# Performance work log

Measured on AMD Instinct MI355X. Metric: run time of the kernel, lower is better.

Reference implementation:

```python
import jax, jax.numpy as jnp
import numpy as np

N, E, D_IN, D_H, N_CLS, N_GRAPHS = 50000, 1600000, 128, 64, 10, 64
NEG_SLOPE = 0.2


def _glorot(key, shape):
    fan_in = shape[0]
    return (jax.random.normal(key, shape, dtype=jnp.float32) * np.sqrt(1.0 / fan_in)).astype(jnp.float32)


def setup_inputs() -> dict:
    key = jax.random.key(0)
    ks = jax.random.split(key, 20)
    inp = {
        "x": jax.random.normal(ks[0], (N, D_IN), dtype=jnp.float32),
        "edge_index": jax.random.randint(ks[1], (2, E), 0, N, dtype=jnp.int64) if jax.config.jax_enable_x64 else jax.random.randint(ks[1], (2, E), 0, N).astype(jnp.int32),
        "edge_attr": jax.random.uniform(ks[2], (E, 1), dtype=jnp.float32),
        "batch": jnp.sort(jax.random.randint(ks[3], (N,), 0, N_GRAPHS)),
        # conv1 params
        "Wl1": _glorot(ks[4], (D_IN, D_H)), "bl1": jnp.zeros((D_H,), jnp.float32),
        "Wr1": _glorot(ks[5], (D_IN, D_H)), "br1": jnp.zeros((D_H,), jnp.float32),
        "We1": _glorot(ks[6], (1, D_H)),
        "att1": _glorot(ks[7], (D_H,)),
        "b1": jnp.zeros((D_H,), jnp.float32),
        # conv2 params
        "Wl2": _glorot(ks[8], (D_H, D_H)), "bl2": jnp.zeros((D_H,), jnp.float32),
        "Wr2": _glorot(ks[9], (D_H, D_H)), "br2": jnp.zeros((D_H,), jnp.float32),
        "We2": _glorot(ks[10], (1, D_H)),
        "att2": _glorot(ks[11], (D_H,)),
        "b2": jnp.zeros((D_H,), jnp.float32),
        # classifier
        "Wc": _glorot(ks[12], (D_H, N_CLS)), "bc": jnp.zeros((N_CLS,), jnp.float32),
    }
    return inp


def _segment_softmax(logits, seg, num_segments):
    m = jax.ops.segment_max(logits, seg, num_segments=num_segments)
    z = jnp.exp(logits - m[seg])
    s = jax.ops.segment_sum(z, seg, num_segments=num_segments)
    return z / (s[seg] + 1e-16)


def _gatv2(x, src, dst, eattr, Wl, bl, Wr, br, We, att, b):
    # PyG GATv2Conv, heads=1, add_self_loops=True (fill_value='mean'), eval mode
    xl = x @ Wl + bl  # source-side transform [N, D]
    xr = x @ Wr + br  # target-side transform [N, D]
    loop = jnp.arange(N, dtype=src.dtype)
    src2 = jnp.concatenate([src, loop])
    dst2 = jnp.concatenate([dst, loop])
    loop_attr = jnp.broadcast_to(eattr.mean(axis=0, keepdims=True), (N, eattr.shape[1]))
    ea2 = jnp.concatenate([eattr, loop_attr], axis=0) @ We  # [E+N, D]
    msg = jax.nn.leaky_relu(xl[src2] + xr[dst2] + ea2, NEG_SLOPE)  # [E+N, D]
    logits = msg @ att  # [E+N]
    alpha = _segment_softmax(logits, dst2, N)
    out = jax.ops.segment_sum(xl[src2] * alpha[:, None], dst2, num_segments=N)
    return out + b


def reference(x, edge_index, edge_attr, batch,
              Wl1, bl1, Wr1, br1, We1, att1, b1,
              Wl2, bl2, Wr2, br2, We2, att2, b2,
              Wc, bc):
    src, dst = edge_index[0], edge_index[1]
    h = jax.nn.elu(_gatv2(x, src, dst, edge_attr, Wl1, bl1, Wr1, br1, We1, att1, b1))
    # dropout p=0.2 is identity in eval mode
    h = jax.nn.elu(_gatv2(h, src, dst, edge_attr, Wl2, bl2, Wr2, br2, We2, att2, b2))
    # global mean pool per graph
    sums = jax.ops.segment_sum(h, batch, num_segments=N_GRAPHS)
    counts = jax.ops.segment_sum(jnp.ones((N,), h.dtype), batch, num_segments=N_GRAPHS)
    pooled = sums / jnp.maximum(counts, 1.0)[:, None]  # [G, D_H]
    return pooled @ Wc + bc
```

## Files before the change

### kernel.cpp

```cpp
#include <hip/hip_runtime.h>
#include <hip/hip_fp16.h>
#include <math.h>

#define N_NODES 50000
#define N_EDGES 1600000
#define D_IN 128
#define D_H 64
#define N_CLS 10
#define N_GRAPHS 64
#define NEG_SLOPE 0.2f
#define E2 (N_EDGES + N_NODES)
#define SCAN_BS 256
#define NBLK ((N_NODES + SCAN_BS - 1) / SCAN_BS)

#define NB 25
#define BSH 11
#define CAP 76800
#define HBB 8
#define EPT 8
#define PAD 32
#define SLICES 8
#define SLICE_W (2048 / SLICES)

typedef _Float16 f16x2 __attribute__((ext_vector_type(2)));

__device__ inline f16x2 as_h2(unsigned u) { return __builtin_bit_cast(f16x2, u); }
__device__ inline int h2_as_int(f16x2 v) { return __builtin_bit_cast(int, v); }

__device__ inline f16x2 pk_leaky(f16x2 m, f16x2 ns) {
#if __has_builtin(__builtin_elementwise_max)
    return __builtin_elementwise_max(m, m * ns);
#else
    f16x2 p = m * ns, r;
    r.x = m.x > p.x ? m.x : p.x;
    r.y = m.y > p.y ? m.y : p.y;
    return r;
#endif
}

#if __has_builtin(__builtin_amdgcn_fdot2)
__device__ inline float fdot2a(f16x2 a, f16x2 b, float c) {
    return __builtin_amdgcn_fdot2(a, b, c, false);
}
#else
__device__ inline float fdot2a(f16x2 a, f16x2 b, float c) {
    return fmaf((float)a.x, (float)b.x, fmaf((float)a.y, (float)b.y, c));
}
#endif

__device__ inline float wave_reduce_sum(float v) {
    for (int off = 32; off; off >>= 1) v += __shfl_xor(v, off);
    return v;
}

__global__ void bucket_stage(const int* __restrict__ src, const int* __restrict__ dst,
                             const float* __restrict__ eattr,
                             float* esum, int* bcursor,
                             int2* __restrict__ stg) {
    __shared__ int bcnt[4][32];
    __shared__ int woff[4][32];
    __shared__ float esh[4];
    int t = threadIdx.x;
    int wave = t >> 6;
    if (t < 128) bcnt[t >> 5][t & 31] = 0;
    __syncthreads();
    int e0 = (blockIdx.x * blockDim.x + t) * EPT;
    int ss[EPT], tt[EPT], aa[EPT], r[EPT], b[EPT];
    float v = 0.f;
    bool valid = e0 < N_EDGES;
    if (valid) {
        #pragma unroll
        for (int q = 0; q < EPT / 4; ++q) {
            int4 s4 = *(const int4*)(src + e0 + 4 * q);
            int4 t4 = *(const int4*)(dst + e0 + 4 * q);
            float4 a4 = *(const float4*)(eattr + e0 + 4 * q);
            ss[4*q] = s4.x; ss[4*q+1] = s4.y; ss[4*q+2] = s4.z; ss[4*q+3] = s4.w;
            tt[4*q] = t4.x; tt[4*q+1] = t4.y; tt[4*q+2] = t4.z; tt[4*q+3] = t4.w;
            aa[4*q]   = h2_as_int((f16x2){(_Float16)a4.x, (_Float16)a4.x});
            aa[4*q+1] = h2_as_int((f16x2){(_Float16)a4.y, (_Float16)a4.y});
            aa[4*q+2] = h2_as_int((f16x2){(_Float16)a4.z, (_Float16)a4.z});
            aa[4*q+3] = h2_as_int((f16x2){(_Float16)a4.w, (_Float16)a4.w});
            v += (a4.x + a4.y) + (a4.z + a4.w);
        }
        #pragma unroll
        for (int i = 0; i < EPT; ++i) {
            b[i] = tt[i] >> BSH;
            r[i] = atomicAdd(&bcnt[wave][b[i]], 1);
        }
    }
    v = wave_reduce_sum(v);
    if ((t & 63) == 0) esh[wave] = v;
    __syncthreads();
    if (t < NB) {
        int c0 = bcnt[0][t], c1 = bcnt[1][t], c2 = bcnt[2][t], c3 = bcnt[3][t];
        int tot = c0 + c1 + c2 + c3;
        int base = tot ? atomicAdd(&bcursor[t * PAD], tot) : 0;
        woff[0][t] = base;
        woff[1][t] = base + c0;
        woff[2][t] = base + c0 + c1;
        woff[3][t] = base + c0 + c1 + c2;
    }
    if (t == 0) {
        float tot = (esh[0] + esh[1]) + (esh[2] + esh[3]);
        atomicAdd(&esum[(blockIdx.x & 31) * PAD], tot);
    }
    __syncthreads();
    if (valid) {
        #pragma unroll
        for (int i = 0; i < EPT; ++i) {
            int p = b[i] * CAP + woff[wave][b[i]] + r[i];
            stg[p] = make_int2((ss[i] & 0xFFFF) | ((tt[i] & 2047) << 16), aa[i]);
        }
    }
}

__global__ void hist_bucket(const int2* __restrict__ stg, const int* __restrict__ bcursor,
                            int* cnt) {
    __shared__ int hist[2048];
    int b = blockIdx.x / HBB;
    int j = blockIdx.x % HBB;
    for (int i = threadIdx.x; i < 2048; i += 256) hist[i] = 0;
    __syncthreads();
    int n = bcursor[b * PAD];
    const int2* sd = stg + (size_t)b * CAP;
    int per = (n + HBB - 1) / HBB;
    int start = j * per;
    int end = min(start + per, n);
    for (int idx = start + threadIdx.x; idx < end; idx += 256)
        atomicAdd(&hist[(sd[idx].x >> 16) & 2047], 1);
    __syncthreads();
    int nb = b << BSH;
    for (int i = threadIdx.x; i < 2048; i += 256) {
        int c = hist[i];
        if (c) atomicAdd(&cnt[nb + i], c);
    }
}

__global__ void scan_block(const int* __restrict__ cnt, int* __restrict__ row_start,
                           int* __restrict__ partial) {
    __shared__ int sd[SCAN_BS];
    int i = blockIdx.x * SCAN_BS + threadIdx.x;
    int v = (i < N_NODES) ? (cnt[i] + 1) : 0;
    sd[threadIdx.x] = v;
    __syncthreads();
    for (int off = 1; off < SCAN_BS; off <<= 1) {
        int t = (threadIdx.x >= off) ? sd[threadIdx.x - off] : 0;
        __syncthreads();
        sd[threadIdx.x] += t;
        __syncthreads();
    }
    if (i < N_NODES) row_start[i] = sd[threadIdx.x] - v;
    if (threadIdx.x == SCAN_BS - 1) partial[blockIdx.x] = sd[threadIdx.x];
}
__global__ void add_offsets(int* __restrict__ row_start, const int* __restrict__ partial,
                            int* __restrict__ cursor, const float* __restrict__ esum,
                            int2* __restrict__ csr_pack) {
    __shared__ int sp[SCAN_BS];
    int pv = (threadIdx.x < NBLK) ? partial[threadIdx.x] : 0;
    sp[threadIdx.x] = pv;
    __syncthreads();
    for (int off = 1; off < SCAN_BS; off <<= 1) {
        int t = (threadIdx.x >= off) ? sp[threadIdx.x - off] : 0;
        __syncthreads();
        sp[threadIdx.x] += t;
        __syncthreads();
    }
    float es = 0.f;
    #pragma unroll
    for (int jj = 0; jj < 32; ++jj) es += esum[jj * PAD];
    float esm = es * (1.0f / N_EDGES);
    int ebits = h2_as_int((f16x2){(_Float16)esm, (_Float16)esm});
    int base = (blockIdx.x == 0) ? 0 : sp[blockIdx.x - 1];
    int i = blockIdx.x * SCAN_BS + threadIdx.x;
    if (i < N_NODES) {
        int r = row_start[i] + base;
        row_start[i] = r;
        csr_pack[r] = make_int2(i, ebits);
        cursor[i] = r + 1;
    }
    if (i == 0) row_start[N_NODES] = E2;
}

__global__ __launch_bounds__(1024) void scatter_slice(
                              const int2* __restrict__ stg,
                              const int* __restrict__ bcursor,
                              const int* __restrict__ row_start,
                              int2* __restrict__ csr_pack) {
    __shared__ int lcur[SLICE_W];
    int b = blockIdx.x & 31;
    int m = blockIdx.x >> 5;
    if (b >= NB) return;
    int nbase = (b << BSH) + m * SLICE_W;
    for (int i = threadIdx.x; i < SLICE_W; i += 1024) {
        int node = nbase + i;
        lcur[i] = (node < N_NODES) ? row_start[node] + 1 : 0;
    }
    __syncthreads();
    int n = bcursor[b * PAD];
    const int4* sd4 = (const int4*)(stg + (size_t)b * CAP);
    int n4 = n >> 1;
    int lo = m * SLICE_W, hi = lo + SLICE_W;
    for (int base4 = 0; base4 < n4; base4 += 4096) {
        int4 e[4];
        int idx[4];
        #pragma unroll
        for (int j = 0; j < 4; ++j) {
            idx[j] = base4 + j * 1024 + (int)threadIdx.x;
            if (idx[j] < n4) e[j] = sd4[idx[j]];
        }
        #pragma unroll
        for (int j = 0; j < 4; ++j) {
            if (idx[j] < n4) {
                int dl0 = (e[j].x >> 16) & 2047;
                if (dl0 >= lo && dl0 < hi) {
                    int q = atomicAdd(&lcur[dl0 - lo], 1);
                    csr_pack[q] = make_int2(e[j].x & 0xFFFF, e[j].y);
                }
                int dl1 = (e[j].z >> 16) & 2047;
                if (dl1 >= lo && dl1 < hi) {
                    int q = atomicAdd(&lcur[dl1 - lo], 1);
                    csr_pack[q] = make_int2(e[j].z & 0xFFFF, e[j].w);
                }
            }
        }
    }
    if ((n & 1) && threadIdx.x == 0) {
        int2 e = stg[(size_t)b * CAP + n - 1];
        int dl = (e.x >> 16) & 2047;
        if (dl >= lo && dl < hi) {
            int q = atomicAdd(&lcur[dl - lo], 1);
            csr_pack[q] = make_int2(e.x & 0xFFFF, e.y);
        }
    }
}

template<int K>
__global__ __launch_bounds__(256) void linear_dual_k(
                              const float* __restrict__ x,
                              const float* __restrict__ Wl, const float* __restrict__ bl,
                              const float* __restrict__ Wr, const float* __restrict__ br,
                              __half* __restrict__ xl, __half* __restrict__ xr) {
    const int TN = 32;
    const int NPW = TN / 4;
    __shared__ float xs[TN * K];
    int t = threadIdx.x;
    int nb = blockIdx.x * TN;
    int rem = N_NODES - nb;
    int tot4 = (rem >= TN ? TN : rem) * (K / 4);
    const float4* xg = (const float4*)(x + (size_t)nb * K);
    float4* xs4 = (float4*)xs;
    for (int i = t; i < tot4; i += 256) xs4[i] = xg[i];
    __syncthreads();
    int wave = t >> 6, d = t & 63;
    int n0 = wave * NPW;
    float blv = bl[d], brv = br[d];
    float al[NPW], ar[NPW];
    #pragma unroll
    for (int i = 0; i < NPW; ++i) { al[i] = blv; ar[i] = brv; }
    #pragma unroll 2
    for (int k4 = 0; k4 < K / 4; ++k4) {
        int kb = k4 * 4;
        float wl[4], wr[4];
        #pragma unroll
        for (int q = 0; q < 4; ++q) {
            wl[q] = Wl[(kb + q) * D_H + d];
            wr[q] = Wr[(kb + q) * D_H + d];
        }
        #pragma unroll
        for (int i = 0; i < NPW; ++i) {
            float4 xv = *(const float4*)&xs[(n0 + i) * K + kb];
            al[i] = fmaf(xv.x, wl[0], al[i]);
            al[i] = fmaf(xv.y, wl[1], al[i]);
            al[i] = fmaf(xv.z, wl[2], al[i]);
            al[i] = fmaf(xv.w, wl[3], al[i]);
            ar[i] = fmaf(xv.x, wr[0], ar[i]);
            ar[i] = fmaf(xv.y, wr[1], ar[i]);
            ar[i] = fmaf(xv.z, wr[2], ar[i]);
            ar[i] = fmaf(xv.w, wr[3], ar[i]);
        }
    }
    #pragma unroll
    for (int i = 0; i < NPW; ++i) {
        int g = nb + n0 + i;
        if (g < N_NODES) {
            xl[(size_t)g * D_H + d] = __float2half(al[i]);
            xr[(size_t)g * D_H + d] = __float2half(ar[i]);
        }
    }
}

__global__ __launch_bounds__(256) void gat_fused(
        const int* __restrict__ row_start, const int2* __restrict__ csr_pack,
        const __half* __restrict__ xl, const __half* __restrict__ xr,
        const float* __restrict__ We, const float* __restrict__ att,
        const float* __restrict__ b, float* __restrict__ out) {
    int lane = threadIdx.x & 63;
    int g = lane >> 3;
    int s = lane & 7;
    int wid = blockIdx.x * (blockDim.x >> 6) + (threadIdx.x >> 6);
    int node = wid * 8 + g;
    bool nv = node < N_NODES;
    int nodec = nv ? node : 0;
    int fb = s * 8;
    float4 wea = *(const float4*)(We + fb), web = *(const float4*)(We + fb + 4);
    float4 ata = *(const float4*)(att + fb), atb = *(const float4*)(att + fb + 4);
    f16x2 we[4] = {{(_Float16)wea.x, (_Float16)wea.y}, {(_Float16)wea.z, (_Float16)wea.w},
                   {(_Float16)web.x, (_Float16)web.y}, {(_Float16)web.z, (_Float16)web.w}};
    f16x2 at[4] = {{(_Float16)ata.x, (_Float16)ata.y}, {(_Float16)ata.z, (_Float16)ata.w},
                   {(_Float16)atb.x, (_Float16)atb.y}, {(_Float16)atb.z, (_Float16)atb.w}};
    int4 xru = *(const int4*)(xr + (size_t)nodec * D_H + fb);
    f16x2 xr4[4] = {as_h2((unsigned)xru.x), as_h2((unsigned)xru.y),
                    as_h2((unsigned)xru.z), as_h2((unsigned)xru.w)};
    const f16x2 ns = {(_Float16)NEG_SLOPE, (_Float16)NEG_SLOPE};
    int j0 = 0, j1 = 0;
    if (nv) { j0 = row_start[node]; j1 = row_start[node + 1]; }

    float S = 0.f;
    float acc[8] = {0.f, 0.f, 0.f, 0.f, 0.f, 0.f, 0.f, 0.f};

    for (int i0 = j0; i0 < j1; i0 += 4) {
        int2 pk[4]; int4 qk[4]; bool vk[4];
        #pragma unroll
        for (int k = 0; k < 4; ++k) {
            vk[k] = (i0 + k) < j1;
            int c = vk[k] ? (i0 + k) : i0;
            pk[k] = csr_pack[c];
        }
        #pragma unroll
        for (int k = 0; k < 4; ++k)
            qk[k] = *(const int4*)(xl + (size_t)pk[k].x * D_H + fb);
        float t[4];
        #pragma unroll
        for (int k = 0; k < 4; ++k) {
            f16x2 a2 = as_h2((unsigned)pk[k].y);
            f16x2 r0 = as_h2((unsigned)qk[k].x), r1 = as_h2((unsigned)qk[k].y);
            f16x2 r2 = as_h2((unsigned)qk[k].z), r3 = as_h2((unsigned)qk[k].w);
            f16x2 m0 = a2 * we[0] + (r0 + xr4[0]);
            f16x2 m1 = a2 * we[1] + (r1 + xr4[1]);
            f16x2 m2 = a2 * we[2] + (r2 + xr4[2]);
            f16x2 m3 = a2 * we[3] + (r3 + xr4[3]);
            m0 = pk_leaky(m0, ns); m1 = pk_leaky(m1, ns);
            m2 = pk_leaky(m2, ns); m3 = pk_leaky(m3, ns);
            t[k] = fdot2a(m3, at[3], fdot2a(m2, at[2],
                   fdot2a(m1, at[1], fdot2a(m0, at[0], 0.f))));
        }
        #pragma unroll
        for (int off = 1; off <= 4; off <<= 1) {
            t[0] += __shfl_xor(t[0], off);
            t[1] += __shfl_xor(t[1], off);
            t[2] += __shfl_xor(t[2], off);
            t[3] += __shfl_xor(t[3], off);
        }
        #pragma unroll
        for (int k = 0; k < 4; ++k) {
            float z = vk[k] ? __expf(t[k]) : 0.f;
            S += z;
            f16x2 r0 = as_h2((unsigned)qk[k].x), r1 = as_h2((unsigned)qk[k].y);
            f16x2 r2 = as_h2((unsigned)qk[k].z), r3 = as_h2((unsigned)qk[k].w);
            acc[0] = fmaf(z, (float)r0.x, acc[0]);
            acc[1] = fmaf(z, (float)r0.y, acc[1]);
            acc[2] = fmaf(z, (float)r1.x, acc[2]);
            acc[3] = fmaf(z, (float)r1.y, acc[3]);
            acc[4] = fmaf(z, (float)r2.x, acc[4]);
            acc[5] = fmaf(z, (float)r2.y, acc[5]);
            acc[6] = fmaf(z, (float)r3.x, acc[6]);
            acc[7] = fmaf(z, (float)r3.y, acc[7]);
        }
    }

    if (nv) {
        float4 ba = *(const float4*)(b + fb), bb = *(const float4*)(b + fb + 4);
        float bq[8] = {ba.x, ba.y, ba.z, ba.w, bb.x, bb.y, bb.z, bb.w};
        float inv = 1.f / (S + 1e-16f);
        float h[8];
        #pragma unroll
        for (int j = 0; j < 8; ++j) {
            float v = fmaf(acc[j], inv, bq[j]);
            h[j] = v > 0.f ? v : expm1f(v);
        }
        *(float4*)(out + (size_t)node * D_H + fb)     = make_float4(h[0], h[1], h[2], h[3]);
        *(float4*)(out + (size_t)node * D_H + fb + 4) = make_float4(h[4], h[5], h[6], h[7]);
    }
}

__global__ void pool(const float* __restrict__ h, const int* __restrict__ batch,
                     float* __restrict__ pooled, float* __restrict__ counts) {
    const int CHUNK = 32;
    int base = blockIdx.x * CHUNK;
    int d = threadIdx.x;
    float accv = 0.f; int cur_g = -1; int cnt = 0;
    for (int i = 0; i < CHUNK; ++i) {
        int n = base + i;
        if (n >= N_NODES) break;
        int g = batch[n];
        if (g != cur_g) {
            if (cur_g >= 0) {
                atomicAdd(&pooled[cur_g * D_H + d], accv);
                if (d == 0) atomicAdd(&counts[cur_g], (float)cnt);
            }
            cur_g = g; accv = 0.f; cnt = 0;
        }
        accv += h[(size_t)n * D_H + d];
        cnt++;
    }
    if (cur_g >= 0) {
        atomicAdd(&pooled[cur_g * D_H + d], accv);
        if (d == 0) atomicAdd(&counts[cur_g], (float)cnt);
    }
}

__global__ void classify(const float* __restrict__ pooled, const float* __restrict__ counts,
                         const float* __restrict__ Wc, const float* __restrict__ bc,
                         float* __restrict__ out) {
    int tid = threadIdx.x;
    int g = tid / N_CLS, c = tid % N_CLS;
    if (g >= N_GRAPHS) return;
    float inv = 1.0f / fmaxf(counts[g], 1.0f);
    float a = bc[c];
    for (int k = 0; k < D_H; ++k)
        a = fmaf(pooled[g * D_H + k] * inv, Wc[k * N_CLS + c], a);
    out[g * N_CLS + c] = a;
}

extern "C" void kernel_launch(void* const* d_in, const int* in_sizes, int n_in,
                              void* d_out, int out_size, void* d_ws, size_t ws_size,
                              hipStream_t stream) {
    const float* x     = (const float*)d_in[0];
    const int*   ei    = (const int*)d_in[1];
    const float* eattr = (const float*)d_in[2];
    const int*   batch = (const int*)d_in[3];
    const float *Wl1 = (const float*)d_in[4],  *bl1 = (const float*)d_in[5];
    const float *Wr1 = (const float*)d_in[6],  *br1 = (const float*)d_in[7];
    const float *We1 = (const float*)d_in[8],  *att1 = (const float*)d_in[9];
    const float *b1  = (const float*)d_in[10];
    const float *Wl2 = (const float*)d_in[11], *bl2 = (const float*)d_in[12];
    const float *Wr2 = (const float*)d_in[13], *br2 = (const float*)d_in[14];
    const float *We2 = (const float*)d_in[15], *att2 = (const float*)d_in[16];
    const float *b2  = (const float*)d_in[17];
    const float *Wc  = (const float*)d_in[18], *bc = (const float*)d_in[19];
    float* out = (float*)d_out;

    const int* src = ei;
    const int* dst = ei + N_EDGES;

    char* base = (char*)d_ws;
    int2*  stg     = (int2*)base;
    __half* xl     = (__half*)base;
    __half* xr     = xl + (size_t)N_NODES * D_H;
    float* h       = (float*)(xr + (size_t)N_NODES * D_H);
    int2*  csr_pack = (int2*)(base + (size_t)NB * CAP * 16);
    int*   row_start = (int*)(csr_pack + E2);
    int*   cnt     = row_start + N_NODES + 1;
    float* esum    = (float*)(cnt + N_NODES);
    int*   bcursor = (int*)(esum + 32 * PAD);
    int*   cursor  = bcursor + NB * PAD;
    int*   partial = cursor + N_NODES;
    float* pooled  = (float*)(partial + NBLK);
    float* counts  = pooled + N_GRAPHS * D_H;

    int gat_blocks = (N_NODES + 31) / 32;
    int lin_blocks = (N_NODES + 31) / 32;

    hipMemsetAsync(cnt, 0, (N_NODES + 32 * PAD + NB * PAD) * sizeof(int), stream);
    hipMemsetAsync(pooled, 0, (N_GRAPHS * D_H + N_GRAPHS) * sizeof(float), stream);

    bucket_stage<<<(N_EDGES / EPT + 255) / 256, 256, 0, stream>>>(
        src, dst, eattr, esum, bcursor, stg);
    hist_bucket<<<NB * HBB, 256, 0, stream>>>(stg, bcursor, cnt);
    scan_block<<<NBLK, SCAN_BS, 0, stream>>>(cnt, row_start, partial);
    add_offsets<<<NBLK, SCAN_BS, 0, stream>>>(row_start, partial, cursor, esum, csr_pack);
    scatter_slice<<<SLICES * 32, 1024, 0, stream>>>(stg, bcursor, row_start, csr_pack);

    linear_dual_k<D_IN><<<lin_blocks, 256, 0, stream>>>(x, Wl1, bl1, Wr1, br1, xl, xr);
    gat_fused<<<gat_blocks, 256, 0, stream>>>(row_start, csr_pack, xl, xr, We1, att1, b1, h);

    linear_dual_k<D_H><<<lin_blocks, 256, 0, stream>>>(h, Wl2, bl2, Wr2, br2, xl, xr);
    gat_fused<<<gat_blocks, 256, 0, stream>>>(row_start, csr_pack, xl, xr, We2, att2, b2, h);

    pool<<<(N_NODES + 31) / 32, 64, 0, stream>>>(h, batch, pooled, counts);
    classify<<<1, 640, 0, stream>>>(pooled, counts, Wc, bc, out);
}
```

Measured before the change: 333.8 us.

## Sort nodes by in-degree to balance GAT wavefront work

Adds a degree histogram, scan and placement pass that produces a node order grouped by in-degree, and makes the GAT aggregation kernel process nodes in that order. Each wavefront handles eight nodes at once, so grouping nodes of similar degree is meant to cut idle lanes from divergent loop trip counts. The cost is three extra small kernel launches, an indirect node lookup, and scattered output and xr accesses in place of contiguous ones. Degrees are Poisson around 33 here, so the imbalance being removed is modest.

Measured after the change: 343.5 us. 2.9% more time.

```diff
diff --git a/kernel.cpp b/kernel.cpp
--- a/kernel.cpp
+++ b/kernel.cpp
@@ -21,6 +21,7 @@
 #define PAD 32
 #define SLICES 8
 #define SLICE_W (2048 / SLICES)
+#define DBINS 128
 
 typedef _Float16 f16x2 __attribute__((ext_vector_type(2)));
 
@@ -179,6 +180,59 @@
         cursor[i] = r + 1;
     }
     if (i == 0) row_start[N_NODES] = E2;
+}
+
+__global__ void deg_hist(const int* __restrict__ row_start, int* __restrict__ dbin) {
+    __shared__ int lh[DBINS];
+    int t = threadIdx.x;
+    for (int i = t; i < DBINS; i += 256) lh[i] = 0;
+    __syncthreads();
+    int i = blockIdx.x * 256 + t;
+    if (i < N_NODES) {
+        int d = min(row_start[i + 1] - row_start[i], DBINS - 1);
+        atomicAdd(&lh[d], 1);
+    }
+    __syncthreads();
+    for (int j = t; j < DBINS; j += 256) {
+        int c = lh[j];
+        if (c) atomicAdd(&dbin[j * PAD], c);
+    }
+}
+__global__ void deg_scan(const int* __restrict__ dbin, int* __restrict__ dcur) {
+    __shared__ int sd[DBINS];
+    int t = threadIdx.x;
+    int v = dbin[t * PAD];
+    sd[t] = v;
+    __syncthreads();
+    for (int off = 1; off < DBINS; off <<= 1) {
+        int u = (t >= off) ? sd[t - off] : 0;
+        __syncthreads();
+        sd[t] += u;
+        __syncthreads();
+    }
+    dcur[t * PAD] = sd[t] - v;
+}
+__global__ void deg_place(const int* __restrict__ row_start, int* __restrict__ dcur,
+                          int* __restrict__ order) {
+    __shared__ int lh[DBINS];
+    __shared__ int lbase[DBINS];
+    int t = threadIdx.x;
+    for (int i = t; i < DBINS; i += 256) lh[i] = 0;
+    __syncthreads();
+    int i = blockIdx.x * 256 + t;
+    int d = 0, r = 0;
+    bool v = i < N_NODES;
+    if (v) {
+        d = min(row_start[i + 1] - row_start[i], DBINS - 1);
+        r = atomicAdd(&lh[d], 1);
+    }
+    __syncthreads();
+    for (int j = t; j < DBINS; j += 256) {
+        int c = lh[j];
+        lbase[j] = c ? atomicAdd(&dcur[j * PAD], c) : 0;
+    }
+    __syncthreads();
+    if (v) order[lbase[d] + r] = i;
 }
 
 __global__ __launch_bounds__(1024) void scatter_slice(
@@ -291,6 +345,7 @@
 
 __global__ __launch_bounds__(256) void gat_fused(
         const int* __restrict__ row_start, const int2* __restrict__ csr_pack,
+        const int* __restrict__ order,
         const __half* __restrict__ xl, const __half* __restrict__ xr,
         const float* __restrict__ We, const float* __restrict__ att,
         const float* __restrict__ b, float* __restrict__ out) {
@@ -298,9 +353,9 @@
     int g = lane >> 3;
     int s = lane & 7;
     int wid = blockIdx.x * (blockDim.x >> 6) + (threadIdx.x >> 6);
-    int node = wid * 8 + g;
-    bool nv = node < N_NODES;
-    int nodec = nv ? node : 0;
+    int idx = wid * 8 + g;
+    bool nv = idx < N_NODES;
+    int node = nv ? order[idx] : 0;
     int fb = s * 8;
     float4 wea = *(const float4*)(We + fb), web = *(const float4*)(We + fb + 4);
     float4 ata = *(const float4*)(att + fb), atb = *(const float4*)(att + fb + 4);
@@ -308,7 +363,7 @@
                    {(_Float16)web.x, (_Float16)web.y}, {(_Float16)web.z, (_Float16)web.w}};
     f16x2 at[4] = {{(_Float16)ata.x, (_Float16)ata.y}, {(_Float16)ata.z, (_Float16)ata.w},
                    {(_Float16)atb.x, (_Float16)atb.y}, {(_Float16)atb.z, (_Float16)atb.w}};
-    int4 xru = *(const int4*)(xr + (size_t)nodec * D_H + fb);
+    int4 xru = *(const int4*)(xr + (size_t)node * D_H + fb);
     f16x2 xr4[4] = {as_h2((unsigned)xru.x), as_h2((unsigned)xru.y),
                     as_h2((unsigned)xru.z), as_h2((unsigned)xru.w)};
     const f16x2 ns = {(_Float16)NEG_SLOPE, (_Float16)NEG_SLOPE};
@@ -323,7 +378,7 @@
         #pragma unroll
         for (int k = 0; k < 4; ++k) {
             vk[k] = (i0 + k) < j1;
-            int c = vk[k] ? (i0 + k) : i0;
+            int c = vk[k] ? (i0 + k) : j0;
             pk[k] = csr_pack[c];
         }
         #pragma unroll
@@ -457,25 +512,32 @@
     int*   partial = cursor + N_NODES;
     float* pooled  = (float*)(partial + NBLK);
     float* counts  = pooled + N_GRAPHS * D_H;
+    int*   dbin    = (int*)(counts + N_GRAPHS);
+    int*   dcur    = dbin + DBINS * PAD;
+    int*   order   = dcur + DBINS * PAD;
 
     int gat_blocks = (N_NODES + 31) / 32;
     int lin_blocks = (N_NODES + 31) / 32;
 
     hipMemsetAsync(cnt, 0, (N_NODES + 32 * PAD + NB * PAD) * sizeof(int), stream);
-    hipMemsetAsync(pooled, 0, (N_GRAPHS * D_H + N_GRAPHS) * sizeof(float), stream);
+    hipMemsetAsync(pooled, 0,
+                   (N_GRAPHS * D_H + N_GRAPHS + DBINS * PAD) * sizeof(float), stream);
 
     bucket_stage<<<(N_EDGES / EPT + 255) / 256, 256, 0, stream>>>(
         src, dst, eattr, esum, bcursor, stg);
     hist_bucket<<<NB * HBB, 256, 0, stream>>>(stg, bcursor, cnt);
     scan_block<<<NBLK, SCAN_BS, 0, stream>>>(cnt, row_start, partial);
     add_offsets<<<NBLK, SCAN_BS, 0, stream>>>(row_start, partial, cursor, esum, csr_pack);
+    deg_hist<<<NBLK, 256, 0, stream>>>(row_start, dbin);
+    deg_scan<<<1, DBINS, 0, stream>>>(dbin, dcur);
+    deg_place<<<NBLK, 256, 0, stream>>>(row_start, dcur, order);
     scatter_slice<<<SLICES * 32, 1024, 0, stream>>>(stg, bcursor, row_start, csr_pack);
 
     linear_dual_k<D_IN><<<lin_blocks, 256, 0, stream>>>(x, Wl1, bl1, Wr1, br1, xl, xr);
-    gat_fused<<<gat_blocks, 256, 0, stream>>>(row_start, csr_pack, xl, xr, We1, att1, b1, h);
+    gat_fused<<<gat_blocks, 256, 0, stream>>>(row_start, csr_pack, order, xl, xr, We1, att1, b1, h);
 
     linear_dual_k<D_H><<<lin_blocks, 256, 0, stream>>>(h, Wl2, bl2, Wr2, br2, xl, xr);
-    gat_fused<<<gat_blocks, 256, 0, stream>>>(row_start, csr_pack, xl, xr, We2, att2, b2, h);
+    gat_fused<<<gat_blocks, 256, 0, stream>>>(row_start, csr_pack, order, xl, xr, We2, att2, b2, h);
 
     pool<<<(N_NODES + 31) / 32, 64, 0, stream>>>(h, batch, pooled, counts);
     classify<<<1, 640, 0, stream>>>(pooled, counts, Wc, bc, out);
```

## Compute dual node linear transforms with fp16 MFMA instructions

Applied to the files above, without the earlier changes.

Replaces the scalar-FMA dual linear kernel with one that converts a 64-node tile of inputs and transposed Wl/Wr weights to fp16 in shared memory. Each wave then computes the outputs for 16 nodes with 16x16x16 f16 MFMA instructions, one accumulator per 16-column tile of the combined 128 outputs. This cuts ALU work in the dense projections, but every block reloads and converts the full weight matrices, and the inputs lose precision from fp32 to fp16.

Result: faster. 307.9 us (-7.8%).

```diff
diff --git a/kernel.cpp b/kernel.cpp
--- a/kernel.cpp
+++ b/kernel.cpp
@@ -23,6 +23,8 @@
 #define SLICE_W (2048 / SLICES)
 
 typedef _Float16 f16x2 __attribute__((ext_vector_type(2)));
+typedef _Float16 f16x4 __attribute__((ext_vector_type(4)));
+typedef float    fv4   __attribute__((ext_vector_type(4)));
 
 __device__ inline f16x2 as_h2(unsigned u) { return __builtin_bit_cast(f16x2, u); }
 __device__ inline int h2_as_int(f16x2 v) { return __builtin_bit_cast(int, v); }
@@ -235,57 +237,92 @@
 }
 
 template<int K>
-__global__ __launch_bounds__(256) void linear_dual_k(
-                              const float* __restrict__ x,
-                              const float* __restrict__ Wl, const float* __restrict__ bl,
-                              const float* __restrict__ Wr, const float* __restrict__ br,
-                              __half* __restrict__ xl, __half* __restrict__ xr) {
-    const int TN = 32;
-    const int NPW = TN / 4;
-    __shared__ float xs[TN * K];
+__global__ __launch_bounds__(256) void linear_dual_mfma(
+        const float* __restrict__ x,
+        const float* __restrict__ Wl, const float* __restrict__ bl,
+        const float* __restrict__ Wr, const float* __restrict__ br,
+        __half* __restrict__ xl, __half* __restrict__ xr) {
+    const int KS = K + 4;
+    __shared__ _Float16 Xh[64 * KS];
+    __shared__ _Float16 Wt[128 * KS];
     int t = threadIdx.x;
-    int nb = blockIdx.x * TN;
-    int rem = N_NODES - nb;
-    int tot4 = (rem >= TN ? TN : rem) * (K / 4);
-    const float4* xg = (const float4*)(x + (size_t)nb * K);
-    float4* xs4 = (float4*)xs;
-    for (int i = t; i < tot4; i += 256) xs4[i] = xg[i];
-    __syncthreads();
-    int wave = t >> 6, d = t & 63;
-    int n0 = wave * NPW;
-    float blv = bl[d], brv = br[d];
-    float al[NPW], ar[NPW];
-    #pragma unroll
-    for (int i = 0; i < NPW; ++i) { al[i] = blv; ar[i] = brv; }
-    #pragma unroll 2
-    for (int k4 = 0; k4 < K / 4; ++k4) {
-        int kb = k4 * 4;
-        float wl[4], wr[4];
-        #pragma unroll
-        for (int q = 0; q < 4; ++q) {
-            wl[q] = Wl[(kb + q) * D_H + d];
-            wr[q] = Wr[(kb + q) * D_H + d];
-        }
-        #pragma unroll
-        for (int i = 0; i < NPW; ++i) {
-            float4 xv = *(const float4*)&xs[(n0 + i) * K + kb];
-            al[i] = fmaf(xv.x, wl[0], al[i]);
-            al[i] = fmaf(xv.y, wl[1], al[i]);
-            al[i] = fmaf(xv.z, wl[2], al[i]);
-            al[i] = fmaf(xv.w, wl[3], al[i]);
-            ar[i] = fmaf(xv.x, wr[0], ar[i]);
-            ar[i] = fmaf(xv.y, wr[1], ar[i]);
-            ar[i] = fmaf(xv.z, wr[2], ar[i]);
-            ar[i] = fmaf(xv.w, wr[3], ar[i]);
-        }
-    }
-    #pragma unroll
-    for (int i = 0; i < NPW; ++i) {
-        int g = nb + n0 + i;
-        if (g < N_NODES) {
-            xl[(size_t)g * D_H + d] = __float2half(al[i]);
-            xr[(size_t)g * D_H + d] = __float2half(ar[i]);
-        }
+    int nb = blockIdx.x * 64;
+    for (int i = t; i < 64 * (K / 4); i += 256) {
+        int n = i / (K / 4), k0 = (i % (K / 4)) * 4;
+        float4 v = (nb + n < N_NODES) ? *(const float4*)(x + (size_t)(nb + n) * K + k0)
+                                      : make_float4(0.f, 0.f, 0.f, 0.f);
+        f16x4 h = {(_Float16)v.x, (_Float16)v.y, (_Float16)v.z, (_Float16)v.w};
+        *(f16x4*)&Xh[n * KS + k0] = h;
+    }
+    for (int i = t; i < K * 64; i += 256) {
+        int k = i >> 6, c = i & 63;
+        Wt[c * KS + k] = (_Float16)Wl[i];
+    }
+    for (int i = t; i < K * 64; i += 256) {
+        int k = i >> 6, c = i & 63;
+        Wt[(c + 64) * KS + k] = (_Float16)Wr[i];
+    }
+    __syncthreads();
+
+    int w = t >> 6, lane = t & 63;
+    int np = lane & 15;
+    int g  = lane >> 4;
+    int node = nb + w * 16 + np;
+    const _Float16* xrow = &Xh[(w * 16 + np) * KS];
+    fv4 acc0 = {0.f,0.f,0.f,0.f}, acc1 = {0.f,0.f,0.f,0.f};
+    fv4 acc2 = {0.f,0.f,0.f,0.f}, acc3 = {0.f,0.f,0.f,0.f};
+    fv4 acc4 = {0.f,0.f,0.f,0.f}, acc5 = {0.f,0.f,0.f,0.f};
+    fv4 acc6 = {0.f,0.f,0.f,0.f}, acc7 = {0.f,0.f,0.f,0.f};
+
+#if __has_builtin(__builtin_amdgcn_mfma_f32_16x16x16f16)
+    for (int k0 = 0; k0 < K; k0 += 16) {
+        f16x4 bf = *(const f16x4*)&xrow[k0 + 4 * g];
+        f16x4 a0 = *(const f16x4*)&Wt[(0 * 16 + np) * KS + k0 + 4 * g];
+        f16x4 a1 = *(const f16x4*)&Wt[(1 * 16 + np) * KS + k0 + 4 * g];
+        f16x4 a2 = *(const f16x4*)&Wt[(2 * 16 + np) * KS + k0 + 4 * g];
+        f16x4 a3 = *(const f16x4*)&Wt[(3 * 16 + np) * KS + k0 + 4 * g];
+        f16x4 a4 = *(const f16x4*)&Wt[(4 * 16 + np) * KS + k0 + 4 * g];
+        f16x4 a5 = *(const f16x4*)&Wt[(5 * 16 + np) * KS + k0 + 4 * g];
+        f16x4 a6 = *(const f16x4*)&Wt[(6 * 16 + np) * KS + k0 + 4 * g];
+        f16x4 a7 = *(const f16x4*)&Wt[(7 * 16 + np) * KS + k0 + 4 * g];
+        acc0 = __builtin_amdgcn_mfma_f32_16x16x16f16(a0, bf, acc0, 0, 0, 0);
+        acc1 = __builtin_amdgcn_mfma_f32_16x16x16f16(a1, bf, acc1, 0, 0, 0);
+        acc2 = __builtin_amdgcn_mfma_f32_16x16x16f16(a2, bf, acc2, 0, 0, 0);
+        acc3 = __builtin_amdgcn_mfma_f32_16x16x16f16(a3, bf, acc3, 0, 0, 0);
+        acc4 = __builtin_amdgcn_mfma_f32_16x16x16f16(a4, bf, acc4, 0, 0, 0);
+        acc5 = __builtin_amdgcn_mfma_f32_16x16x16f16(a5, bf, acc5, 0, 0, 0);
+        acc6 = __builtin_amdgcn_mfma_f32_16x16x16f16(a6, bf, acc6, 0, 0, 0);
+        acc7 = __builtin_amdgcn_mfma_f32_16x16x16f16(a7, bf, acc7, 0, 0, 0);
+    }
+#else
+    {
+        fv4* accs[8] = {&acc0,&acc1,&acc2,&acc3,&acc4,&acc5,&acc6,&acc7};
+        for (int ct = 0; ct < 8; ++ct)
+            for (int j = 0; j < 4; ++j) {
+                float s = 0.f;
+                const _Float16* wrow = &Wt[(ct * 16 + 4 * g + j) * KS];
+                for (int k = 0; k < K; ++k) s += (float)wrow[k] * (float)xrow[k];
+                (*accs[ct])[j] = s;
+            }
+    }
+#endif
+
+    if (node < N_NODES) {
+        #define EMIT(CT, ACC)                                                        \
+        {                                                                            \
+            const float* bp = ((CT) < 4) ? (bl + (CT) * 16 + 4 * g)                  \
+                                         : (br + ((CT) - 4) * 16 + 4 * g);           \
+            float4 bv = *(const float4*)bp;                                          \
+            f16x4 o = {(_Float16)(ACC[0] + bv.x), (_Float16)(ACC[1] + bv.y),         \
+                       (_Float16)(ACC[2] + bv.z), (_Float16)(ACC[3] + bv.w)};        \
+            __half* dst = ((CT) < 4)                                                 \
+                ? (xl + (size_t)node * D_H + (CT) * 16 + 4 * g)                      \
+                : (xr + (size_t)node * D_H + ((CT) - 4) * 16 + 4 * g);               \
+            *(f16x4*)dst = o;                                                        \
+        }
+        EMIT(0, acc0) EMIT(1, acc1) EMIT(2, acc2) EMIT(3, acc3)
+        EMIT(4, acc4) EMIT(5, acc5) EMIT(6, acc6) EMIT(7, acc7)
+        #undef EMIT
     }
 }
 
@@ -459,7 +496,7 @@
     float* counts  = pooled + N_GRAPHS * D_H;
 
     int gat_blocks = (N_NODES + 31) / 32;
-    int lin_blocks = (N_NODES + 31) / 32;
+    int mfma_blocks = (N_NODES + 63) / 64;
 
     hipMemsetAsync(cnt, 0, (N_NODES + 32 * PAD + NB * PAD) * sizeof(int), stream);
     hipMemsetAsync(pooled, 0, (N_GRAPHS * D_H + N_GRAPHS) * sizeof(float), stream);
@@ -471,10 +508,10 @@
     add_offsets<<<NBLK, SCAN_BS, 0, stream>>>(row_start, partial, cursor, esum, csr_pack);
     scatter_slice<<<SLICES * 32, 1024, 0, stream>>>(stg, bcursor, row_start, csr_pack);
 
-    linear_dual_k<D_IN><<<lin_blocks, 256, 0, stream>>>(x, Wl1, bl1, Wr1, br1, xl, xr);
+    linear_dual_mfma<D_IN><<<mfma_blocks, 256, 0, stream>>>(x, Wl1, bl1, Wr1, br1, xl, xr);
     gat_fused<<<gat_blocks, 256, 0, stream>>>(row_start, csr_pack, xl, xr, We1, att1, b1, h);
 
-    linear_dual_k<D_H><<<lin_blocks, 256, 0, stream>>>(h, Wl2, bl2, Wr2, br2, xl, xr);
+    linear_dual_mfma<D_H><<<mfma_blocks, 256, 0, stream>>>(h, Wl2, bl2, Wr2, br2, xl, xr);
     gat_fused<<<gat_blocks, 256, 0, stream>>>(row_start, csr_pack, xl, xr, We2, att2, b2, h);
 
     pool<<<(N_NODES + 31) / 32, 64, 0, stream>>>(h, batch, pooled, counts);
```
